# Kernel tuning notes

Measured on AMD Instinct MI355X. Metric: run time of the kernel, lower is better.

## Reference

```python
import jax, jax.numpy as jnp
import numpy as np

TRANS = np.array([[0.704,0.079,0.035,0.072,0.041,0.038],
                  [0.127,0.493,0.13,0.073,0.09,0.08],
                  [0.084,0.172,0.428,0.097,0.153,0.081],
                  [0.279,0.12,0.12,0.36,0.062,0.092],
                  [0.068,0.124,0.206,0.072,0.447,0.092],
                  [0.074,0.176,0.12,0.132,0.124,0.408]], dtype=np.float32)
ALPHA = 0.9


def setup_inputs() -> dict:
    key = jax.random.key(0)
    k1, = jax.random.split(key, 1)
    B, T, C = 8192, 1024, 6
    feats = jax.random.normal(k1, (B, T, C), dtype=jnp.float32)
    alpha = jnp.array([ALPHA], dtype=jnp.float32)
    transitions = jnp.asarray(TRANS)
    return {"feats": feats, "alpha": alpha, "transitions": transitions}


def reference(feats, alpha, transitions):
    # feats: [B, T, C]; alpha: [1]; transitions: [C, C]
    a = jax.nn.sigmoid(alpha)                      # [1]
    Tn = jax.nn.softmax(transitions, axis=-1)      # [C, C], row-normalized

    def step(state, cur):
        # transfer_energy[b, j] = logsumexp_i(state[b, i] * Tn[i, j])
        scores = state[:, :, None] * Tn[None, :, :]           # [B, C, C]
        te = jax.scipy.special.logsumexp(scores, axis=1)      # [B, C]
        new_state = a * cur + (1.0 - a) * te                  # [B, C]
        return new_state, new_state

    feats_tm = jnp.swapaxes(feats, 0, 1)           # [T, B, C] time-major
    init = feats_tm[0]                             # first step: state = feats[:, 0]
    _, rest = jax.lax.scan(step, init, feats_tm[1:])
    out = jnp.concatenate([init[None], rest], axis=0)  # [T, B, C]
    return jnp.swapaxes(out, 0, 1)                 # [B, T, C]
```

## Files before the change

### kernel.cpp

```cpp
#include <hip/hip_runtime.h>

#define T_STEPS 1024
#define CC 6
#define NCHUNK 8
#define CHUNK (T_STEPS / NCHUNK)
#define WARM 16
#define KBUF 16
#define NBLK (CHUNK / KBUF)
#define GPAD 100
#define LOG2E 1.4426950408889634f
#define LN2   0.6931471805599453f

__device__ __forceinline__ float fexp2(float x) {
#if __has_builtin(__builtin_amdgcn_exp2f)
    return __builtin_amdgcn_exp2f(x);
#else
    return exp2f(x);
#endif
}

__device__ __forceinline__ float flog2(float x) {
#if __has_builtin(__builtin_amdgcn_logf)
    return __builtin_amdgcn_logf(x);
#else
    return log2f(x);
#endif
}

__global__ __launch_bounds__(256, 8) void transfer_kernel(
    const float* __restrict__ feats,
    const float* __restrict__ alpha,
    const float* __restrict__ trans,
    float* __restrict__ out, int B)
{
    __shared__ float sbuf[32 * GPAD];

    int tid = blockIdx.x * blockDim.x + threadIdx.x;
    int g   = tid >> 3;
    int gb  = (threadIdx.x >> 3);
    int j   = tid & 7;
    int jl  = j < CC ? j : (CC - 1);
    if (g >= B * NCHUNK) return;

    int b = g % B;
    int c = g / B;

    float a  = 1.0f / (1.0f + fexp2(-alpha[0] * LOG2E));
    float c1 = (1.0f - a) * LN2;

    float tcol[CC];
#pragma unroll
    for (int i = 0; i < CC; ++i) {
        float rs = 0.0f;
#pragma unroll
        for (int k = 0; k < CC; ++k)
            rs += fexp2(trans[i * CC + k] * LOG2E);
        tcol[i] = (fexp2(trans[i * CC + jl] * LOG2E) / rs) * LOG2E;
    }

    const float* fb = feats + (size_t)b * T_STEPS * CC;
    float*       ob = out   + (size_t)b * T_STEPS * CC;
    float*       sg = &sbuf[gb * GPAD];

#define STEP_LDS(PSLOT, xv)                                              \
    do {                                                                 \
        float2 s01 = *reinterpret_cast<const float2*>(&sg[(PSLOT) * CC + 0]); \
        float2 s23 = *reinterpret_cast<const float2*>(&sg[(PSLOT) * CC + 2]); \
        float2 s45 = *reinterpret_cast<const float2*>(&sg[(PSLOT) * CC + 4]); \
        float sum;                                                       \
        sum  = fexp2(s01.x * tcol[0]);                                   \
        sum += fexp2(s01.y * tcol[1]);                                   \
        sum += fexp2(s23.x * tcol[2]);                                   \
        sum += fexp2(s23.y * tcol[3]);                                   \
        sum += fexp2(s45.x * tcol[4]);                                   \
        sum += fexp2(s45.y * tcol[5]);                                   \
        state = a * (xv) + c1 * flog2(sum);                              \
    } while (0)

    int t0 = c * CHUNK;
    float state;

    if (c != 0) {
        int tw = t0 - WARM;
        state  = fb[tw * CC + jl];
        sg[0 * CC + jl] = state;
#pragma unroll
        for (int w = 1; w < WARM; ++w) {
            float x = fb[(tw + w) * CC + jl];
            STEP_LDS(w - 1, x);
            sg[w * CC + jl] = state;
        }
    }

#pragma unroll 1
    for (int kb = 0; kb < NBLK; ++kb) {
        int tbase = t0 + kb * KBUF;

#pragma unroll
        for (int kk = 0; kk < KBUF; ++kk) {
            float x = fb[(tbase + kk) * CC + jl];
            if (kk == 0) {
                if (kb == 0 && c == 0) {
                    state = x;
                } else {
                    STEP_LDS(KBUF - 1, x);
                }
            } else {
                STEP_LDS(kk - 1, x);
            }
            sg[kk * CC + jl] = state;
        }

        int obase = tbase * CC;
#pragma unroll
        for (int k = 0; k < 3; ++k) {
            int idx = (k * 8 + j) * 4;
            float4 v = *reinterpret_cast<const float4*>(&sg[idx]);
            *reinterpret_cast<float4*>(&ob[obase + idx]) = v;
        }
    }
#undef STEP_LDS
}

extern "C" void kernel_launch(void* const* d_in, const int* in_sizes, int n_in,
                              void* d_out, int out_size, void* d_ws, size_t ws_size,
                              hipStream_t stream) {
    const float* feats = (const float*)d_in[0];
    const float* alpha = (const float*)d_in[1];
    const float* trans = (const float*)d_in[2];
    float* out = (float*)d_out;

    int B = in_sizes[0] / (T_STEPS * CC);

    int threads = B * NCHUNK * 8;
    int block   = 256;
    int grid    = (threads + block - 1) / block;

    hipLaunchKernelGGL(transfer_kernel, dim3(grid), dim3(block), 0, stream,
                       feats, alpha, trans, out, B);
}
```

Before: 359.3 us.

## Process two independent time chunks per thread group to add ILP

Each 8-lane group now runs two time chunks (A and B) of the same batch row, interleaving their recurrences so two independent dependency chains hide exp/log and LDS latency. The number of thread groups is halved, LDS per block doubles, and the launch bounds drop to 4 blocks per CU to allow more registers. The cost is fewer resident waves, since TLP is traded for ILP, plus the chunk-0 path no longer needs a warmup for its A half.

```diff
diff --git a/kernel.cpp b/kernel.cpp
--- a/kernel.cpp
+++ b/kernel.cpp
@@ -3,6 +3,7 @@
 #define T_STEPS 1024
 #define CC 6
 #define NCHUNK 8
+#define NQ (NCHUNK / 2)
 #define CHUNK (T_STEPS / NCHUNK)
 #define WARM 16
 #define KBUF 16
@@ -27,23 +28,23 @@
 #endif
 }
 
-__global__ __launch_bounds__(256, 8) void transfer_kernel(
+__global__ __launch_bounds__(256, 4) void transfer_kernel(
     const float* __restrict__ feats,
     const float* __restrict__ alpha,
     const float* __restrict__ trans,
     float* __restrict__ out, int B)
 {
-    __shared__ float sbuf[32 * GPAD];
+    __shared__ float sbuf[32 * 2 * GPAD];
 
     int tid = blockIdx.x * blockDim.x + threadIdx.x;
     int g   = tid >> 3;
     int gb  = (threadIdx.x >> 3);
     int j   = tid & 7;
     int jl  = j < CC ? j : (CC - 1);
-    if (g >= B * NCHUNK) return;
+    if (g >= B * NQ) return;
 
     int b = g % B;
-    int c = g / B;
+    int q = g / B;
 
     float a  = 1.0f / (1.0f + fexp2(-alpha[0] * LOG2E));
     float c1 = (1.0f - a) * LN2;
@@ -60,63 +61,76 @@
 
     const float* fb = feats + (size_t)b * T_STEPS * CC;
     float*       ob = out   + (size_t)b * T_STEPS * CC;
-    float*       sg = &sbuf[gb * GPAD];
+    float* sgA = &sbuf[gb * 2 * GPAD];
+    float* sgB = sgA + GPAD;
 
-#define STEP_LDS(PSLOT, xv)                                              \
-    do {                                                                 \
-        float2 s01 = *reinterpret_cast<const float2*>(&sg[(PSLOT) * CC + 0]); \
-        float2 s23 = *reinterpret_cast<const float2*>(&sg[(PSLOT) * CC + 2]); \
-        float2 s45 = *reinterpret_cast<const float2*>(&sg[(PSLOT) * CC + 4]); \
-        float sum;                                                       \
-        sum  = fexp2(s01.x * tcol[0]);                                   \
-        sum += fexp2(s01.y * tcol[1]);                                   \
-        sum += fexp2(s23.x * tcol[2]);                                   \
-        sum += fexp2(s23.y * tcol[3]);                                   \
-        sum += fexp2(s45.x * tcol[4]);                                   \
-        sum += fexp2(s45.y * tcol[5]);                                   \
-        state = a * (xv) + c1 * flog2(sum);                              \
+#define STEP_LDS(SG, PSLOT, ST, xv)                                       \
+    do {                                                                  \
+        float2 s01 = *reinterpret_cast<const float2*>(&(SG)[(PSLOT) * CC + 0]); \
+        float2 s23 = *reinterpret_cast<const float2*>(&(SG)[(PSLOT) * CC + 2]); \
+        float2 s45 = *reinterpret_cast<const float2*>(&(SG)[(PSLOT) * CC + 4]); \
+        float sum;                                                        \
+        sum  = fexp2(s01.x * tcol[0]);                                    \
+        sum += fexp2(s01.y * tcol[1]);                                    \
+        sum += fexp2(s23.x * tcol[2]);                                    \
+        sum += fexp2(s23.y * tcol[3]);                                    \
+        sum += fexp2(s45.x * tcol[4]);                                    \
+        sum += fexp2(s45.y * tcol[5]);                                    \
+        (ST) = a * (xv) + c1 * flog2(sum);                                \
     } while (0)
 
-    int t0 = c * CHUNK;
-    float state;
+    int t0A = (2 * q) * CHUNK;
+    int t0B = t0A + CHUNK;
+    float stA, stB;
 
-    if (c != 0) {
-        int tw = t0 - WARM;
-        state  = fb[tw * CC + jl];
-        sg[0 * CC + jl] = state;
+    if (q != 0) {
+        int twA = t0A - WARM, twB = t0B - WARM;
+        stA = fb[twA * CC + jl];  sgA[jl] = stA;
+        stB = fb[twB * CC + jl];  sgB[jl] = stB;
 #pragma unroll
         for (int w = 1; w < WARM; ++w) {
-            float x = fb[(tw + w) * CC + jl];
-            STEP_LDS(w - 1, x);
-            sg[w * CC + jl] = state;
+            float xA = fb[(twA + w) * CC + jl];
+            float xB = fb[(twB + w) * CC + jl];
+            STEP_LDS(sgA, w - 1, stA, xA);  sgA[w * CC + jl] = stA;
+            STEP_LDS(sgB, w - 1, stB, xB);  sgB[w * CC + jl] = stB;
+        }
+    } else {
+        int twB = t0B - WARM;
+        stB = fb[twB * CC + jl];  sgB[jl] = stB;
+#pragma unroll
+        for (int w = 1; w < WARM; ++w) {
+            float xB = fb[(twB + w) * CC + jl];
+            STEP_LDS(sgB, w - 1, stB, xB);  sgB[w * CC + jl] = stB;
         }
     }
 
 #pragma unroll 1
     for (int kb = 0; kb < NBLK; ++kb) {
-        int tbase = t0 + kb * KBUF;
+        int tbA = t0A + kb * KBUF;
+        int tbB = t0B + kb * KBUF;
 
 #pragma unroll
         for (int kk = 0; kk < KBUF; ++kk) {
-            float x = fb[(tbase + kk) * CC + jl];
-            if (kk == 0) {
-                if (kb == 0 && c == 0) {
-                    state = x;
-                } else {
-                    STEP_LDS(KBUF - 1, x);
-                }
+            float xA = fb[(tbA + kk) * CC + jl];
+            float xB = fb[(tbB + kk) * CC + jl];
+            int ps = (kk == 0) ? (KBUF - 1) : (kk - 1);
+            if (kk == 0 && kb == 0 && q == 0) {
+                stA = xA;
             } else {
-                STEP_LDS(kk - 1, x);
+                STEP_LDS(sgA, ps, stA, xA);
             }
-            sg[kk * CC + jl] = state;
+            sgA[kk * CC + jl] = stA;
+            STEP_LDS(sgB, ps, stB, xB);
+            sgB[kk * CC + jl] = stB;
         }
 
-        int obase = tbase * CC;
 #pragma unroll
         for (int k = 0; k < 3; ++k) {
             int idx = (k * 8 + j) * 4;
-            float4 v = *reinterpret_cast<const float4*>(&sg[idx]);
-            *reinterpret_cast<float4*>(&ob[obase + idx]) = v;
+            float4 vA = *reinterpret_cast<const float4*>(&sgA[idx]);
+            *reinterpret_cast<float4*>(&ob[tbA * CC + idx]) = vA;
+            float4 vB = *reinterpret_cast<const float4*>(&sgB[idx]);
+            *reinterpret_cast<float4*>(&ob[tbB * CC + idx]) = vB;
         }
     }
 #undef STEP_LDS
@@ -132,7 +146,7 @@
 
     int B = in_sizes[0] / (T_STEPS * CC);
 
-    int threads = B * NCHUNK * 8;
+    int threads = B * NQ * 8;
     int block   = 256;
     int grid    = (threads + block - 1) / block;
 
```

After: 371.1 us. 1.03x slower.

## Give each thread a full batch-chunk state in registers and double chunk count

Applied to the files above, without the earlier changes.

Replaces the 8-lane-per-sequence mapping with LDS state exchange by one thread per (batch, chunk) that holds all six state values and a 16-step input buffer in registers. Input and output are moved with per-thread float4 bursts, and the time axis is split into 16 chunks instead of 8 to keep enough threads. This removes idle lanes and LDS traffic but raises register pressure, worsens global coalescing, and increases the relative warm-up recomputation per chunk.

```diff
diff --git a/kernel.cpp b/kernel.cpp
--- a/kernel.cpp
+++ b/kernel.cpp
@@ -2,12 +2,12 @@
 
 #define T_STEPS 1024
 #define CC 6
-#define NCHUNK 8
+#define NCHUNK 16
 #define CHUNK (T_STEPS / NCHUNK)
 #define WARM 16
 #define KBUF 16
 #define NBLK (CHUNK / KBUF)
-#define GPAD 100
+#define BUFN (KBUF * CC)
 #define LOG2E 1.4426950408889634f
 #define LN2   0.6931471805599453f
 
@@ -27,99 +27,104 @@
 #endif
 }
 
-__global__ __launch_bounds__(256, 8) void transfer_kernel(
+__global__ __launch_bounds__(256, 1) void transfer_kernel(
     const float* __restrict__ feats,
     const float* __restrict__ alpha,
     const float* __restrict__ trans,
     float* __restrict__ out, int B)
 {
-    __shared__ float sbuf[32 * GPAD];
-
     int tid = blockIdx.x * blockDim.x + threadIdx.x;
-    int g   = tid >> 3;
-    int gb  = (threadIdx.x >> 3);
-    int j   = tid & 7;
-    int jl  = j < CC ? j : (CC - 1);
-    if (g >= B * NCHUNK) return;
-
-    int b = g % B;
-    int c = g / B;
+    if (tid >= B * NCHUNK) return;
+    int b = tid % B;
+    int c = tid / B;
 
     float a  = 1.0f / (1.0f + fexp2(-alpha[0] * LOG2E));
     float c1 = (1.0f - a) * LN2;
 
-    float tcol[CC];
+    float tm[CC][CC];
 #pragma unroll
     for (int i = 0; i < CC; ++i) {
         float rs = 0.0f;
 #pragma unroll
         for (int k = 0; k < CC; ++k)
             rs += fexp2(trans[i * CC + k] * LOG2E);
-        tcol[i] = (fexp2(trans[i * CC + jl] * LOG2E) / rs) * LOG2E;
+        float inv = LOG2E / rs;
+#pragma unroll
+        for (int jj = 0; jj < CC; ++jj)
+            tm[i][jj] = fexp2(trans[i * CC + jj] * LOG2E) * inv;
     }
 
     const float* fb = feats + (size_t)b * T_STEPS * CC;
     float*       ob = out   + (size_t)b * T_STEPS * CC;
-    float*       sg = &sbuf[gb * GPAD];
 
-#define STEP_LDS(PSLOT, xv)                                              \
-    do {                                                                 \
-        float2 s01 = *reinterpret_cast<const float2*>(&sg[(PSLOT) * CC + 0]); \
-        float2 s23 = *reinterpret_cast<const float2*>(&sg[(PSLOT) * CC + 2]); \
-        float2 s45 = *reinterpret_cast<const float2*>(&sg[(PSLOT) * CC + 4]); \
-        float sum;                                                       \
-        sum  = fexp2(s01.x * tcol[0]);                                   \
-        sum += fexp2(s01.y * tcol[1]);                                   \
-        sum += fexp2(s23.x * tcol[2]);                                   \
-        sum += fexp2(s23.y * tcol[3]);                                   \
-        sum += fexp2(s45.x * tcol[4]);                                   \
-        sum += fexp2(s45.y * tcol[5]);                                   \
-        state = a * (xv) + c1 * flog2(sum);                              \
+    float st[CC];
+    float buf[BUFN];
+
+#define LOADBURST(T0)                                                        \
+    do {                                                                     \
+        _Pragma("unroll")                                                    \
+        for (int k = 0; k < BUFN / 4; ++k) {                                 \
+            float4 v = *reinterpret_cast<const float4*>(&fb[(T0) * CC + 4 * k]); \
+            buf[4 * k + 0] = v.x; buf[4 * k + 1] = v.y;                      \
+            buf[4 * k + 2] = v.z; buf[4 * k + 3] = v.w;                      \
+        }                                                                    \
+    } while (0)
+
+#define STEPB(KK)                                                         \
+    do {                                                                  \
+        float ns[CC];                                                     \
+        _Pragma("unroll")                                                 \
+        for (int jj = 0; jj < CC; ++jj) {                                 \
+            float sum;                                                    \
+            sum  = fexp2(st[0] * tm[0][jj]);                              \
+            sum += fexp2(st[1] * tm[1][jj]);                              \
+            sum += fexp2(st[2] * tm[2][jj]);                              \
+            sum += fexp2(st[3] * tm[3][jj]);                              \
+            sum += fexp2(st[4] * tm[4][jj]);                              \
+            sum += fexp2(st[5] * tm[5][jj]);                              \
+            ns[jj] = a * buf[(KK) * CC + jj] + c1 * flog2(sum);           \
+        }                                                                 \
+        _Pragma("unroll")                                                 \
+        for (int jj = 0; jj < CC; ++jj) {                                 \
+            st[jj] = ns[jj];                                              \
+            buf[(KK) * CC + jj] = ns[jj];                                 \
+        }                                                                 \
     } while (0)
 
     int t0 = c * CHUNK;
-    float state;
 
     if (c != 0) {
-        int tw = t0 - WARM;
-        state  = fb[tw * CC + jl];
-        sg[0 * CC + jl] = state;
+        LOADBURST(t0 - WARM);
 #pragma unroll
-        for (int w = 1; w < WARM; ++w) {
-            float x = fb[(tw + w) * CC + jl];
-            STEP_LDS(w - 1, x);
-            sg[w * CC + jl] = state;
-        }
+        for (int jj = 0; jj < CC; ++jj) st[jj] = buf[jj];
+#pragma unroll
+        for (int w = 1; w < WARM; ++w) STEPB(w);
     }
 
 #pragma unroll 1
     for (int kb = 0; kb < NBLK; ++kb) {
         int tbase = t0 + kb * KBUF;
+        LOADBURST(tbase);
+
+        if (kb == 0 && c == 0) {
+#pragma unroll
+            for (int jj = 0; jj < CC; ++jj) st[jj] = buf[jj];
+#pragma unroll
+            for (int kk = 1; kk < KBUF; ++kk) STEPB(kk);
+        } else {
+#pragma unroll
+            for (int kk = 0; kk < KBUF; ++kk) STEPB(kk);
+        }
 
 #pragma unroll
-        for (int kk = 0; kk < KBUF; ++kk) {
-            float x = fb[(tbase + kk) * CC + jl];
-            if (kk == 0) {
-                if (kb == 0 && c == 0) {
-                    state = x;
-                } else {
-                    STEP_LDS(KBUF - 1, x);
-                }
-            } else {
-                STEP_LDS(kk - 1, x);
-            }
-            sg[kk * CC + jl] = state;
-        }
-
-        int obase = tbase * CC;
-#pragma unroll
-        for (int k = 0; k < 3; ++k) {
-            int idx = (k * 8 + j) * 4;
-            float4 v = *reinterpret_cast<const float4*>(&sg[idx]);
-            *reinterpret_cast<float4*>(&ob[obase + idx]) = v;
+        for (int k = 0; k < BUFN / 4; ++k) {
+            float4 v = make_float4(buf[4 * k + 0], buf[4 * k + 1],
+                                   buf[4 * k + 2], buf[4 * k + 3]);
+            *reinterpret_cast<float4*>(&ob[tbase * CC + 4 * k]) = v;
         }
     }
-#undef STEP_LDS
+#undef STEPB
+#undef LOADBURST
 }
 
 extern "C" void kernel_launch(void* const* d_in, const int* in_sizes, int n_in,
@@ -132,7 +137,7 @@
 
     int B = in_sizes[0] / (T_STEPS * CC);
 
-    int threads = B * NCHUNK * 8;
+    int threads = B * NCHUNK;
     int block   = 256;
     int grid    = (threads + block - 1) / block;
 
```

New measurement: 395.5 us. 1.1x slower.
